# Performance work log

Hardware: AMD Instinct MI355X
Metric: run time of the kernel (lower is better)

The kernel has to match this reference:

```python
import jax, jax.numpy as jnp
import numpy as np

N_NODES = 100000


def _gcn_norm(edge_index, n):
    # PyG GCNConv: add self-loops, symmetric normalization D^-1/2 (A+I) D^-1/2
    loops = jnp.arange(n, dtype=edge_index.dtype)
    src = jnp.concatenate([edge_index[0], loops])
    dst = jnp.concatenate([edge_index[1], loops])
    deg = jax.ops.segment_sum(jnp.ones_like(dst, dtype=jnp.float32), dst, num_segments=n)
    dis = jnp.where(deg > 0, jax.lax.rsqrt(jnp.maximum(deg, 1.0)), 0.0)
    norm = dis[src] * dis[dst]  # [E + n]
    return src, dst, norm


def _gcn_layer(h, W, b, src, dst, norm, n):
    h = h @ W                              # dense projection [n, out]
    msg = h[src] * norm[:, None]           # gather + scale   [E+n, out]
    agg = jax.ops.segment_sum(msg, dst, num_segments=n)  # scatter-add
    return agg + b


def setup_inputs() -> dict:
    key = jax.random.key(0)
    ks = jax.random.split(key, 8)
    n, f, h, d, e = N_NODES, 256, 128, 64, 1600000
    x = jax.random.normal(ks[0], (n, f), dtype=jnp.float32)
    edge_index = jax.random.randint(ks[1], (2, e), 0, n, dtype=jnp.int64)
    s1 = 1.0 / np.sqrt(f)
    s2 = 1.0 / np.sqrt(h)
    return {
        "x": x,
        "edge_index": edge_index,
        "W1": jax.random.normal(ks[2], (f, h), dtype=jnp.float32) * s1,
        "b1": jnp.zeros((h,), dtype=jnp.float32),
        "Wmu": jax.random.normal(ks[3], (h, d), dtype=jnp.float32) * s2,
        "bmu": jnp.zeros((d,), dtype=jnp.float32),
        "Wvar": jax.random.normal(ks[4], (h, d), dtype=jnp.float32) * s2,
        "bvar": jnp.zeros((d,), dtype=jnp.float32),
    }


def reference(x, edge_index, W1, b1, Wmu, bmu, Wvar, bvar):
    n = x.shape[0]
    src, dst, norm = _gcn_norm(edge_index, n)
    h = jax.nn.relu(_gcn_layer(x, W1, b1, src, dst, norm, n))
    mu = _gcn_layer(h, Wmu, bmu, src, dst, norm, n)
    sigma = _gcn_layer(h, Wvar, bvar, src, dst, norm, n)
    return mu, sigma
```

## Files before the change

### kernel.cpp

```cpp
#include <hip/hip_runtime.h>


#define HID 128
#define DOUT 64
#define NB_SHIFT 8
#define CHUNK 8192
#define MAXNB 400

typedef _Float16 half_t;
typedef half_t f16x4 __attribute__((ext_vector_type(4)));
typedef half_t f16x8 __attribute__((ext_vector_type(8)));
typedef float  f32x4 __attribute__((ext_vector_type(4)));


__global__ __launch_bounds__(256) void bincount_kernel(const int* __restrict__ dst,
                                                       int* __restrict__ counts,
                                                       int E, int nblocks, int NB) {
    __shared__ int hist[MAXNB];
    const int b = blockIdx.x;
    for (int t = threadIdx.x; t < NB; t += 256) hist[t] = 0;
    __syncthreads();
    const int beg = b * CHUNK;
    const int end = min(E, beg + CHUNK);
    for (int e = beg + threadIdx.x; e < end; e += 256)
        atomicAdd(&hist[dst[e] >> NB_SHIFT], 1);
    __syncthreads();
    for (int t = threadIdx.x; t < NB; t += 256)
        counts[t * nblocks + b] = hist[t];
}

__global__ __launch_bounds__(256) void scan1_kernel(const int* __restrict__ in,
                                                    int* __restrict__ out,
                                                    int* __restrict__ bsum, int n) {
    __shared__ int s[256];
    int b = blockIdx.x, t = threadIdx.x;
    int base = b * 1024 + t * 4;
    int v0 = 0, v1 = 0, v2 = 0, v3 = 0;
    if (base + 0 < n) v0 = in[base + 0];
    if (base + 1 < n) v1 = in[base + 1];
    if (base + 2 < n) v2 = in[base + 2];
    if (base + 3 < n) v3 = in[base + 3];
    int tsum = v0 + v1 + v2 + v3;
    s[t] = tsum;
    __syncthreads();
    for (int off = 1; off < 256; off <<= 1) {
        int x = (t >= off) ? s[t - off] : 0;
        __syncthreads();
        s[t] += x;
        __syncthreads();
    }
    int excl = s[t] - tsum;
    if (base + 0 < n) out[base + 0] = excl;
    if (base + 1 < n) out[base + 1] = excl + v0;
    if (base + 2 < n) out[base + 2] = excl + v0 + v1;
    if (base + 3 < n) out[base + 3] = excl + v0 + v1 + v2;
    if (t == 255) bsum[b] = s[255];
}

__global__ __launch_bounds__(1024) void scan2_kernel(int* __restrict__ bsum, int nb) {
    __shared__ int s[1024];
    int t = threadIdx.x;
    int v = (t < nb) ? bsum[t] : 0;
    s[t] = v;
    __syncthreads();
    for (int off = 1; off < 1024; off <<= 1) {
        int x = (t >= off) ? s[t - off] : 0;
        __syncthreads();
        s[t] += x;
        __syncthreads();
    }
    if (t < nb) bsum[t] = s[t] - v;
}

__global__ void scan3_kernel(int* __restrict__ out, const int* __restrict__ bsum, int n) {
    int i = blockIdx.x * blockDim.x + threadIdx.x;
    if (i < n) out[i] += bsum[i >> 10];
}

__global__ __launch_bounds__(1024) void binscatter_kernel(const int* __restrict__ src,
                                                          const int* __restrict__ dst,
                                                          const int* __restrict__ offsets,
                                                          int2* __restrict__ binned,
                                                          int E, int nblocks, int NB) {
    __shared__ int  lhist[1024];
    __shared__ int  lbase[1024];
    __shared__ int  cur[1024];
    __shared__ int  goff[MAXNB];
    __shared__ int2 staged[CHUNK];
    const int b = blockIdx.x, t = threadIdx.x;
    const int beg = b * CHUNK;
    const int end = min(E, beg + CHUNK);
    const int ne  = end - beg;

    lhist[t] = 0;
    for (int k = t; k < NB; k += 1024) goff[k] = offsets[k * nblocks + b];
    __syncthreads();

    int2 regs[8];
    #pragma unroll
    for (int j = 0; j < 8; j++) {
        int e = beg + t + j * 1024;
        if (e < end) {
            regs[j] = make_int2(src[e], dst[e]);
            atomicAdd(&lhist[regs[j].y >> NB_SHIFT], 1);
        }
    }
    __syncthreads();

    int hv = lhist[t];
    for (int off = 1; off < 1024; off <<= 1) {
        int x = (t >= off) ? lhist[t - off] : 0;
        __syncthreads();
        lhist[t] += x;
        __syncthreads();
    }
    lbase[t] = lhist[t] - hv;
    cur[t]   = lhist[t] - hv;
    __syncthreads();

    #pragma unroll
    for (int j = 0; j < 8; j++) {
        int e = beg + t + j * 1024;
        if (e < end) {
            int pos = atomicAdd(&cur[regs[j].y >> NB_SHIFT], 1);
            staged[pos] = regs[j];
        }
    }
    __syncthreads();

    #pragma unroll
    for (int j = 0; j < 8; j++) {
        int tt = t + j * 1024;
        if (tt < ne) {
            int2 sd = staged[tt];
            int bkt = sd.y >> NB_SHIFT;
            binned[goff[bkt] + (tt - lbase[bkt])] = sd;
        }
    }
}

__global__ __launch_bounds__(256) void csrbuild_kernel(const int2* __restrict__ binned,
                                                       const int* __restrict__ offsets,
                                                       int* __restrict__ rowptr_end,
                                                       int* __restrict__ colA,
                                                       float* __restrict__ dis,
                                                       int E, int nblocks, int NB, int n) {
    __shared__ int deg[256];
    __shared__ int sc[256];
    __shared__ int cur[256];
    const int b = blockIdx.x;
    const int t = threadIdx.x;
    const int base = offsets[b * nblocks];
    const int bend = (b + 1 < NB) ? offsets[(b + 1) * nblocks] : E;

    deg[t] = 0;
    __syncthreads();
    for (int e = base + t; e < bend; e += 256)
        atomicAdd(&deg[binned[e].y & 255], 1);
    __syncthreads();

    int v = deg[t];
    sc[t] = v;
    __syncthreads();
    for (int off = 1; off < 256; off <<= 1) {
        int x = (t >= off) ? sc[t - off] : 0;
        __syncthreads();
        sc[t] += x;
        __syncthreads();
    }
    int incl = sc[t];
    int node = (b << NB_SHIFT) + t;
    if (node < n) {
        rowptr_end[node] = base + incl;
        dis[node] = rsqrtf((float)v + 1.0f);
    }
    cur[t] = base + incl - v;
    __syncthreads();

    for (int e = base + t; e < bend; e += 256) {
        int2 sd = binned[e];
        int pos = atomicAdd(&cur[sd.y & 255], 1);
        colA[pos] = sd.x;
    }
}

__global__ void w1t_kernel(const float* __restrict__ W1, half_t* __restrict__ W1T) {
    int i = blockIdx.x * blockDim.x + threadIdx.x;
    int k = i >> 7, nn = i & 127;
    W1T[nn * 256 + k] = (half_t)W1[i];
}
__global__ void wcatt_kernel(const float* __restrict__ Wmu, const float* __restrict__ Wvar,
                             half_t* __restrict__ WcatT) {
    int i = blockIdx.x * blockDim.x + threadIdx.x;
    int k = i >> 7, nn = i & 127;
    float v = (nn < DOUT) ? Wmu[k * DOUT + nn] : Wvar[k * DOUT + (nn - DOUT)];
    WcatT[nn * 128 + k] = (half_t)v;
}

__global__ __launch_bounds__(256) void gemm1_mfma(const float* __restrict__ A,
                                                  const half_t* __restrict__ BT,
                                                  const float* __restrict__ dis,
                                                  half_t* __restrict__ C, int M) {
    __shared__ half_t As[64][72];
    __shared__ half_t Bs[128][72];
    const int tid = threadIdx.x;
    const int block_row = blockIdx.x * 64;
    const int wave = tid >> 6, lane = tid & 63;
    const int wm = (wave & 1) * 32, wn = (wave >> 1) * 64;
    const int l16 = lane & 15, quad = lane >> 4;

    f32x4 acc[2][4] = {};
    float4 pa[4];
    f16x8  pb[4];

    #pragma unroll
    for (int i = 0; i < 4; i++) {
        int idx = tid + i * 256;
        int r = idx >> 4, c = idx & 15;
        int row = block_row + r; row = row < M ? row : M - 1;
        pa[i] = ((const float4*)(A + (size_t)row * 256))[c];
    }
    #pragma unroll
    for (int i = 0; i < 4; i++) {
        int idx = tid + i * 256;
        int nr = idx >> 3, kc = idx & 7;
        pb[i] = *(const f16x8*)(BT + (size_t)nr * 256 + kc * 8);
    }

    for (int k0 = 0; k0 < 256; k0 += 64) {
        #pragma unroll
        for (int i = 0; i < 4; i++) {
            int idx = tid + i * 256;
            int r = idx >> 4, c = idx & 15;
            f16x4 hv = { (half_t)pa[i].x, (half_t)pa[i].y, (half_t)pa[i].z, (half_t)pa[i].w };
            *(f16x4*)(&As[r][c * 4]) = hv;
        }
        #pragma unroll
        for (int i = 0; i < 4; i++) {
            int idx = tid + i * 256;
            int nr = idx >> 3, kc = idx & 7;
            *(f16x8*)(&Bs[nr][kc * 8]) = pb[i];
        }
        __syncthreads();

        if (k0 < 192) {
            #pragma unroll
            for (int i = 0; i < 4; i++) {
                int idx = tid + i * 256;
                int r = idx >> 4, c = idx & 15;
                int row = block_row + r; row = row < M ? row : M - 1;
                pa[i] = ((const float4*)(A + (size_t)row * 256 + k0 + 64))[c];
            }
            #pragma unroll
            for (int i = 0; i < 4; i++) {
                int idx = tid + i * 256;
                int nr = idx >> 3, kc = idx & 7;
                pb[i] = *(const f16x8*)(BT + (size_t)nr * 256 + k0 + 64 + kc * 8);
            }
        }

        #pragma unroll
        for (int ks = 0; ks < 2; ks++) {
            f16x8 af[2], bf[4];
            #pragma unroll
            for (int mt = 0; mt < 2; mt++)
                af[mt] = *(const f16x8*)(&As[wm + mt * 16 + l16][ks * 32 + quad * 8]);
            #pragma unroll
            for (int nt = 0; nt < 4; nt++)
                bf[nt] = *(const f16x8*)(&Bs[wn + nt * 16 + l16][ks * 32 + quad * 8]);
            #pragma unroll
            for (int mt = 0; mt < 2; mt++)
                #pragma unroll
                for (int nt = 0; nt < 4; nt++)
                    acc[mt][nt] = __builtin_amdgcn_mfma_f32_16x16x32_f16(af[mt], bf[nt], acc[mt][nt], 0, 0, 0);
        }
        __syncthreads();
    }

    #pragma unroll
    for (int mt = 0; mt < 2; mt++) {
        #pragma unroll
        for (int r = 0; r < 4; r++) {
            int row = block_row + wm + mt * 16 + quad * 4 + r;
            if (row < M) {
                float d = dis[row];
                #pragma unroll
                for (int nt = 0; nt < 4; nt++) {
                    int col = wn + nt * 16 + l16;
                    C[((size_t)(col >> 6) * M + row) * 64 + (col & 63)] = (half_t)(acc[mt][nt][r] * d);
                }
            }
        }
    }
}

__global__ __launch_bounds__(256) void gemm2_mfma(const half_t* __restrict__ A,
                                                  const half_t* __restrict__ BT,
                                                  const float* __restrict__ bmu,
                                                  const float* __restrict__ bvar,
                                                  float* __restrict__ out_mu,
                                                  float* __restrict__ out_sig, int M) {
    __shared__ half_t As[64][72];
    __shared__ half_t Bs[128][72];
    const int tid = threadIdx.x;
    const int block_row = blockIdx.x * 64;
    const int wave = tid >> 6, lane = tid & 63;
    const int wm = (wave & 1) * 32, wn = (wave >> 1) * 64;
    const int l16 = lane & 15, quad = lane >> 4;

    f32x4 acc[2][4] = {};
    f16x8 pa[2], pb[4];

    #pragma unroll
    for (int i = 0; i < 2; i++) {
        int idx = tid + i * 256;
        int r = idx >> 3, kc = idx & 7;
        int row = block_row + r; row = row < M ? row : M - 1;
        pa[i] = *(const f16x8*)(A + (size_t)row * 64 + kc * 8);
    }
    #pragma unroll
    for (int i = 0; i < 4; i++) {
        int idx = tid + i * 256;
        int nr = idx >> 3, kc = idx & 7;
        pb[i] = *(const f16x8*)(BT + (size_t)nr * 128 + kc * 8);
    }

    for (int k0 = 0; k0 < 128; k0 += 64) {
        #pragma unroll
        for (int i = 0; i < 2; i++) {
            int idx = tid + i * 256;
            int r = idx >> 3, kc = idx & 7;
            *(f16x8*)(&As[r][kc * 8]) = pa[i];
        }
        #pragma unroll
        for (int i = 0; i < 4; i++) {
            int idx = tid + i * 256;
            int nr = idx >> 3, kc = idx & 7;
            *(f16x8*)(&Bs[nr][kc * 8]) = pb[i];
        }
        __syncthreads();

        if (k0 < 64) {
            #pragma unroll
            for (int i = 0; i < 2; i++) {
                int idx = tid + i * 256;
                int r = idx >> 3, kc = idx & 7;
                int row = block_row + r; row = row < M ? row : M - 1;
                pa[i] = *(const f16x8*)(A + ((size_t)M + row) * 64 + kc * 8);
            }
            #pragma unroll
            for (int i = 0; i < 4; i++) {
                int idx = tid + i * 256;
                int nr = idx >> 3, kc = idx & 7;
                pb[i] = *(const f16x8*)(BT + (size_t)nr * 128 + 64 + kc * 8);
            }
        }

        #pragma unroll
        for (int ks = 0; ks < 2; ks++) {
            f16x8 af[2], bf[4];
            #pragma unroll
            for (int mt = 0; mt < 2; mt++)
                af[mt] = *(const f16x8*)(&As[wm + mt * 16 + l16][ks * 32 + quad * 8]);
            #pragma unroll
            for (int nt = 0; nt < 4; nt++)
                bf[nt] = *(const f16x8*)(&Bs[wn + nt * 16 + l16][ks * 32 + quad * 8]);
            #pragma unroll
            for (int mt = 0; mt < 2; mt++)
                #pragma unroll
                for (int nt = 0; nt < 4; nt++)
                    acc[mt][nt] = __builtin_amdgcn_mfma_f32_16x16x32_f16(af[mt], bf[nt], acc[mt][nt], 0, 0, 0);
        }
        __syncthreads();
    }

    float bias[4];
    int cols[4];
    #pragma unroll
    for (int nt = 0; nt < 4; nt++) {
        int col = wn + nt * 16 + l16;
        cols[nt] = col;
        bias[nt] = (col < DOUT) ? bmu[col] : bvar[col - DOUT];
    }

    #pragma unroll
    for (int mt = 0; mt < 2; mt++) {
        #pragma unroll
        for (int r = 0; r < 4; r++) {
            int row = block_row + wm + mt * 16 + quad * 4 + r;
            if (row < M) {
                #pragma unroll
                for (int nt = 0; nt < 4; nt++) {
                    int col = cols[nt];
                    float v = acc[mt][nt][r] + bias[nt];
                    if (col < DOUT) out_mu[(size_t)row * DOUT + col] = v;
                    else            out_sig[(size_t)row * DOUT + (col - DOUT)] = v;
                }
            }
        }
    }
}

__device__ __forceinline__ void acc_mix(float& a0, float& a1, float& a2, float& a3,
                                        f16x4 v, float fl) {
    union { f16x4 h; int i[2]; } u; u.h = v;
    asm("v_fma_mix_f32 %0, %1, %2, %0 op_sel_hi:[1,0,0]"
        : "+v"(a0) : "v"(u.i[0]), "v"(fl));
    asm("v_fma_mix_f32 %0, %1, %2, %0 op_sel:[1,0,0] op_sel_hi:[1,0,0]"
        : "+v"(a1) : "v"(u.i[0]), "v"(fl));
    asm("v_fma_mix_f32 %0, %1, %2, %0 op_sel_hi:[1,0,0]"
        : "+v"(a2) : "v"(u.i[1]), "v"(fl));
    asm("v_fma_mix_f32 %0, %1, %2, %0 op_sel:[1,0,0] op_sel_hi:[1,0,0]"
        : "+v"(a3) : "v"(u.i[1]), "v"(fl));
}

template <bool LAYER1>
__global__ __launch_bounds__(256) void agg_kernel(const int* __restrict__ rowptr_end,
                                                  const int* __restrict__ col,
                                                  const float* __restrict__ dis,
                                                  const half_t* __restrict__ hin,
                                                  half_t* __restrict__ hout,
                                                  const float* __restrict__ bias, int n) {
    const int bid   = blockIdx.x;
    const int chunk = (bid >> 2) & 1;
    const int nb4   = (bid >> 3) * 4 + (bid & 3);
    const int node  = nb4 * 16 + (threadIdx.x >> 4);
    if (node >= n) return;
    const int lane16 = threadIdx.x & 15;

    const f16x4* hc = (const f16x4*)(hin + (size_t)chunk * n * 64);

    int beg = (node == 0) ? 0 : rowptr_end[node - 1];
    int end = rowptr_end[node];

    float one = 1.0f;
    float ax = 0.f, ay = 0.f, az = 0.f, aw = 0.f;
    acc_mix(ax, ay, az, aw, hc[(size_t)node * 16 + lane16], one);

    int deg = end - beg;
    if (deg > 0) {
        const int last = end - 1;
        int c[8];
        #pragma unroll
        for (int j = 0; j < 8; j++) c[j] = col[min(beg + j, last)];

        int ng = (deg + 7) >> 3;
        int e = beg;
        for (int g = 0; g < ng; g++) {
            f16x4 v[8];
            #pragma unroll
            for (int j = 0; j < 8; j++) v[j] = hc[(size_t)c[j] * 16 + lane16];

            int enext = e + 8;
            if (g + 1 < ng) {
                #pragma unroll
                for (int j = 0; j < 8; j++) c[j] = col[min(enext + j, last)];
                #pragma unroll
                for (int j = 0; j < 8; j++) acc_mix(ax, ay, az, aw, v[j], one);
            } else {
                int rem = end - e;
                #pragma unroll
                for (int j = 0; j < 8; j++) {
                    float fl = (j < rem) ? 1.0f : 0.0f;
                    acc_mix(ax, ay, az, aw, v[j], fl);
                }
            }
            e = enext;
        }
    }

    float di = dis[node];
    if (LAYER1) {
        const float4 b = ((const float4*)bias)[chunk * 16 + lane16];
        ax = ax * di + b.x; ay = ay * di + b.y; az = az * di + b.z; aw = aw * di + b.w;
        ax = (ax > 0.f ? ax : 0.f) * di;
        ay = (ay > 0.f ? ay : 0.f) * di;
        az = (az > 0.f ? az : 0.f) * di;
        aw = (aw > 0.f ? aw : 0.f) * di;
    } else {
        ax *= di; ay *= di; az *= di; aw *= di;
    }
    f16x4 o = { (half_t)ax, (half_t)ay, (half_t)az, (half_t)aw };
    ((f16x4*)(hout + (size_t)chunk * n * 64))[(size_t)node * 16 + lane16] = o;
}

extern "C" void kernel_launch(void* const* d_in, const int* in_sizes, int n_in,
                              void* d_out, int out_size, void* d_ws, size_t ws_size,
                              hipStream_t stream) {
    const float* x    = (const float*)d_in[0];
    const int*   ei   = (const int*)d_in[1];
    const float* W1   = (const float*)d_in[2];
    const float* b1   = (const float*)d_in[3];
    const float* Wmu  = (const float*)d_in[4];
    const float* bmu  = (const float*)d_in[5];
    const float* Wvar = (const float*)d_in[6];
    const float* bvar = (const float*)d_in[7];

    const int n = in_sizes[0] / 256;
    const int E = in_sizes[1] / 2;
    const int* src = ei;
    const int* dst = ei + E;

    const int NB      = (n + 255) >> NB_SHIFT;
    const int nblocks = (E + CHUNK - 1) / CHUNK;
    const int flat    = NB * nblocks;
    const int nb_scan = (flat + 1023) / 1024;

    char* ws = (char*)d_ws;
    size_t off = 0;
    auto alloc = [&](size_t bytes) { void* p = ws + off; off = (off + bytes + 255) & ~(size_t)255; return p; };
    float*  dis     = (float*) alloc((size_t)n * 4);
    int*    rowptr  = (int*)   alloc((size_t)n * 4);
    int*    counts  = (int*)   alloc((size_t)flat * 4);
    int*    offsets = (int*)   alloc((size_t)flat * 4);
    int*    bsum    = (int*)   alloc((size_t)nb_scan * 4 + 256);
    int2*   binned  = (int2*)  alloc((size_t)E * 8);
    int*    col     = (int*)   alloc((size_t)E * 4);
    half_t* W1T     = (half_t*)alloc((size_t)256 * HID * 2);
    half_t* WcatT   = (half_t*)alloc((size_t)HID * HID * 2);
    half_t* hs      = (half_t*)alloc((size_t)n * HID * 2);
    half_t* h1s     = (half_t*)alloc((size_t)n * HID * 2);
    half_t* agg2    = hs;

    float* out_mu  = (float*)d_out;
    float* out_sig = (float*)d_out + (size_t)n * DOUT;

    bincount_kernel<<<nblocks, 256, 0, stream>>>(dst, counts, E, nblocks, NB);
    scan1_kernel<<<nb_scan, 256, 0, stream>>>(counts, offsets, bsum, flat);
    scan2_kernel<<<1, 1024, 0, stream>>>(bsum, nb_scan);
    scan3_kernel<<<(flat + 255) / 256, 256, 0, stream>>>(offsets, bsum, flat);
    binscatter_kernel<<<nblocks, 1024, 0, stream>>>(src, dst, offsets, binned, E, nblocks, NB);
    csrbuild_kernel<<<NB, 256, 0, stream>>>(binned, offsets, rowptr, col, dis, E, nblocks, NB, n);

    w1t_kernel<<<(256 * HID) / 256, 256, 0, stream>>>(W1, W1T);
    wcatt_kernel<<<(HID * HID) / 256, 256, 0, stream>>>(Wmu, Wvar, WcatT);

    const int aggGrid = ((n + 63) / 64) * 8;
    gemm1_mfma<<<(n + 63) / 64, 256, 0, stream>>>(x, W1T, dis, hs, n);
    agg_kernel<true><<<aggGrid, 256, 0, stream>>>(rowptr, col, dis, hs, h1s, b1, n);
    agg_kernel<false><<<aggGrid, 256, 0, stream>>>(rowptr, col, dis, h1s, agg2, nullptr, n);
    gemm2_mfma<<<(n + 63) / 64, 256, 0, stream>>>(agg2, WcatT, bmu, bvar, out_mu, out_sig, n);
}
```

Measured before the change: 198.7 us.

## Widen aggregation loads to 16 bytes and fold scan/weight-prep launches

The aggregation kernel now has each thread handle 8 half features with 16-byte loads instead of 4 with 8-byte loads, so each 64-feature chunk row is covered by 8 lanes and a block covers 32 nodes instead of 16. The aim is fewer memory transactions per gathered neighbor row and fewer threads issuing per edge. The scan3 fix-up kernel is removed, and the block-sum correction is applied where the offsets are read in binscatter and csrbuild. The two weight-transpose kernels are merged into one launch. Per-thread register use grows with the 8-wide accumulators and loads, which could lower occupancy for the latency-bound gather.

```diff
diff --git a/kernel.cpp b/kernel.cpp
--- a/kernel.cpp
+++ b/kernel.cpp
@@ -72,14 +72,10 @@
     if (t < nb) bsum[t] = s[t] - v;
 }
 
-__global__ void scan3_kernel(int* __restrict__ out, const int* __restrict__ bsum, int n) {
-    int i = blockIdx.x * blockDim.x + threadIdx.x;
-    if (i < n) out[i] += bsum[i >> 10];
-}
-
 __global__ __launch_bounds__(1024) void binscatter_kernel(const int* __restrict__ src,
                                                           const int* __restrict__ dst,
                                                           const int* __restrict__ offsets,
+                                                          const int* __restrict__ bsum,
                                                           int2* __restrict__ binned,
                                                           int E, int nblocks, int NB) {
     __shared__ int  lhist[1024];
@@ -93,7 +89,10 @@
     const int ne  = end - beg;
 
     lhist[t] = 0;
-    for (int k = t; k < NB; k += 1024) goff[k] = offsets[k * nblocks + b];
+    for (int k = t; k < NB; k += 1024) {
+        int idx = k * nblocks + b;
+        goff[k] = offsets[idx] + bsum[idx >> 10];
+    }
     __syncthreads();
 
     int2 regs[8];
@@ -141,6 +140,7 @@
 
 __global__ __launch_bounds__(256) void csrbuild_kernel(const int2* __restrict__ binned,
                                                        const int* __restrict__ offsets,
+                                                       const int* __restrict__ bsum,
                                                        int* __restrict__ rowptr_end,
                                                        int* __restrict__ colA,
                                                        float* __restrict__ dis,
@@ -150,8 +150,11 @@
     __shared__ int cur[256];
     const int b = blockIdx.x;
     const int t = threadIdx.x;
-    const int base = offsets[b * nblocks];
-    const int bend = (b + 1 < NB) ? offsets[(b + 1) * nblocks] : E;
+    const int i0 = b * nblocks;
+    const int base = offsets[i0] + bsum[i0 >> 10];
+    int bend;
+    if (b + 1 < NB) { int i1 = (b + 1) * nblocks; bend = offsets[i1] + bsum[i1 >> 10]; }
+    else            bend = E;
 
     deg[t] = 0;
     __syncthreads();
@@ -184,17 +187,21 @@
     }
 }
 
-__global__ void w1t_kernel(const float* __restrict__ W1, half_t* __restrict__ W1T) {
-    int i = blockIdx.x * blockDim.x + threadIdx.x;
-    int k = i >> 7, nn = i & 127;
-    W1T[nn * 256 + k] = (half_t)W1[i];
-}
-__global__ void wcatt_kernel(const float* __restrict__ Wmu, const float* __restrict__ Wvar,
+__global__ void wprep_kernel(const float* __restrict__ W1,
+                             const float* __restrict__ Wmu,
+                             const float* __restrict__ Wvar,
+                             half_t* __restrict__ W1T,
                              half_t* __restrict__ WcatT) {
     int i = blockIdx.x * blockDim.x + threadIdx.x;
-    int k = i >> 7, nn = i & 127;
-    float v = (nn < DOUT) ? Wmu[k * DOUT + nn] : Wvar[k * DOUT + (nn - DOUT)];
-    WcatT[nn * 128 + k] = (half_t)v;
+    if (i < 256 * HID) {
+        int k = i >> 7, nn = i & 127;
+        W1T[nn * 256 + k] = (half_t)W1[i];
+    } else {
+        int j = i - 256 * HID;
+        int k = j >> 7, nn = j & 127;
+        float v = (nn < DOUT) ? Wmu[k * DOUT + nn] : Wvar[k * DOUT + (nn - DOUT)];
+        WcatT[nn * 128 + k] = (half_t)v;
+    }
 }
 
 __global__ __launch_bounds__(256) void gemm1_mfma(const float* __restrict__ A,
@@ -401,17 +408,15 @@
     }
 }
 
-__device__ __forceinline__ void acc_mix(float& a0, float& a1, float& a2, float& a3,
-                                        f16x4 v, float fl) {
-    union { f16x4 h; int i[2]; } u; u.h = v;
-    asm("v_fma_mix_f32 %0, %1, %2, %0 op_sel_hi:[1,0,0]"
-        : "+v"(a0) : "v"(u.i[0]), "v"(fl));
-    asm("v_fma_mix_f32 %0, %1, %2, %0 op_sel:[1,0,0] op_sel_hi:[1,0,0]"
-        : "+v"(a1) : "v"(u.i[0]), "v"(fl));
-    asm("v_fma_mix_f32 %0, %1, %2, %0 op_sel_hi:[1,0,0]"
-        : "+v"(a2) : "v"(u.i[1]), "v"(fl));
-    asm("v_fma_mix_f32 %0, %1, %2, %0 op_sel:[1,0,0] op_sel_hi:[1,0,0]"
-        : "+v"(a3) : "v"(u.i[1]), "v"(fl));
+__device__ __forceinline__ void acc_mix8(float* a, f16x8 v, float fl) {
+    union { f16x8 h; int i[4]; } u; u.h = v;
+    #pragma unroll
+    for (int k = 0; k < 4; k++) {
+        asm("v_fma_mix_f32 %0, %1, %2, %0 op_sel_hi:[1,0,0]"
+            : "+v"(a[2 * k]) : "v"(u.i[k]), "v"(fl));
+        asm("v_fma_mix_f32 %0, %1, %2, %0 op_sel:[1,0,0] op_sel_hi:[1,0,0]"
+            : "+v"(a[2 * k + 1]) : "v"(u.i[k]), "v"(fl));
+    }
 }
 
 template <bool LAYER1>
@@ -423,19 +428,19 @@
                                                   const float* __restrict__ bias, int n) {
     const int bid   = blockIdx.x;
     const int chunk = (bid >> 2) & 1;
-    const int nb4   = (bid >> 3) * 4 + (bid & 3);
-    const int node  = nb4 * 16 + (threadIdx.x >> 4);
+    const int nb    = (bid >> 3) * 4 + (bid & 3);
+    const int node  = nb * 32 + (threadIdx.x >> 3);
     if (node >= n) return;
-    const int lane16 = threadIdx.x & 15;
-
-    const f16x4* hc = (const f16x4*)(hin + (size_t)chunk * n * 64);
+    const int lane8 = threadIdx.x & 7;
+
+    const f16x8* hc = (const f16x8*)(hin + (size_t)chunk * n * 64);
 
     int beg = (node == 0) ? 0 : rowptr_end[node - 1];
     int end = rowptr_end[node];
 
     float one = 1.0f;
-    float ax = 0.f, ay = 0.f, az = 0.f, aw = 0.f;
-    acc_mix(ax, ay, az, aw, hc[(size_t)node * 16 + lane16], one);
+    float a[8] = {};
+    acc_mix8(a, hc[(size_t)node * 8 + lane8], one);
 
     int deg = end - beg;
     if (deg > 0) {
@@ -447,22 +452,22 @@
         int ng = (deg + 7) >> 3;
         int e = beg;
         for (int g = 0; g < ng; g++) {
-            f16x4 v[8];
-            #pragma unroll
-            for (int j = 0; j < 8; j++) v[j] = hc[(size_t)c[j] * 16 + lane16];
+            f16x8 v[8];
+            #pragma unroll
+            for (int j = 0; j < 8; j++) v[j] = hc[(size_t)c[j] * 8 + lane8];
 
             int enext = e + 8;
             if (g + 1 < ng) {
                 #pragma unroll
                 for (int j = 0; j < 8; j++) c[j] = col[min(enext + j, last)];
                 #pragma unroll
-                for (int j = 0; j < 8; j++) acc_mix(ax, ay, az, aw, v[j], one);
+                for (int j = 0; j < 8; j++) acc_mix8(a, v[j], one);
             } else {
                 int rem = end - e;
                 #pragma unroll
                 for (int j = 0; j < 8; j++) {
                     float fl = (j < rem) ? 1.0f : 0.0f;
-                    acc_mix(ax, ay, az, aw, v[j], fl);
+                    acc_mix8(a, v[j], fl);
                 }
             }
             e = enext;
@@ -471,17 +476,21 @@
 
     float di = dis[node];
     if (LAYER1) {
-        const float4 b = ((const float4*)bias)[chunk * 16 + lane16];
-        ax = ax * di + b.x; ay = ay * di + b.y; az = az * di + b.z; aw = aw * di + b.w;
-        ax = (ax > 0.f ? ax : 0.f) * di;
-        ay = (ay > 0.f ? ay : 0.f) * di;
-        az = (az > 0.f ? az : 0.f) * di;
-        aw = (aw > 0.f ? aw : 0.f) * di;
+        const float4 b0 = ((const float4*)bias)[chunk * 16 + lane8 * 2];
+        const float4 b1 = ((const float4*)bias)[chunk * 16 + lane8 * 2 + 1];
+        float bb[8] = { b0.x, b0.y, b0.z, b0.w, b1.x, b1.y, b1.z, b1.w };
+        #pragma unroll
+        for (int k = 0; k < 8; k++) {
+            float t = a[k] * di + bb[k];
+            a[k] = (t > 0.f ? t : 0.f) * di;
+        }
     } else {
-        ax *= di; ay *= di; az *= di; aw *= di;
-    }
-    f16x4 o = { (half_t)ax, (half_t)ay, (half_t)az, (half_t)aw };
-    ((f16x4*)(hout + (size_t)chunk * n * 64))[(size_t)node * 16 + lane16] = o;
+        #pragma unroll
+        for (int k = 0; k < 8; k++) a[k] *= di;
+    }
+    f16x8 o = { (half_t)a[0], (half_t)a[1], (half_t)a[2], (half_t)a[3],
+                (half_t)a[4], (half_t)a[5], (half_t)a[6], (half_t)a[7] };
+    ((f16x8*)(hout + (size_t)chunk * n * 64))[(size_t)node * 8 + lane8] = o;
 }
 
 extern "C" void kernel_launch(void* const* d_in, const int* in_sizes, int n_in,
@@ -528,14 +537,12 @@
     bincount_kernel<<<nblocks, 256, 0, stream>>>(dst, counts, E, nblocks, NB);
     scan1_kernel<<<nb_scan, 256, 0, stream>>>(counts, offsets, bsum, flat);
     scan2_kernel<<<1, 1024, 0, stream>>>(bsum, nb_scan);
-    scan3_kernel<<<(flat + 255) / 256, 256, 0, stream>>>(offsets, bsum, flat);
-    binscatter_kernel<<<nblocks, 1024, 0, stream>>>(src, dst, offsets, binned, E, nblocks, NB);
-    csrbuild_kernel<<<NB, 256, 0, stream>>>(binned, offsets, rowptr, col, dis, E, nblocks, NB, n);
-
-    w1t_kernel<<<(256 * HID) / 256, 256, 0, stream>>>(W1, W1T);
-    wcatt_kernel<<<(HID * HID) / 256, 256, 0, stream>>>(Wmu, Wvar, WcatT);
-
-    const int aggGrid = ((n + 63) / 64) * 8;
+    binscatter_kernel<<<nblocks, 1024, 0, stream>>>(src, dst, offsets, bsum, binned, E, nblocks, NB);
+    csrbuild_kernel<<<NB, 256, 0, stream>>>(binned, offsets, bsum, rowptr, col, dis, E, nblocks, NB, n);
+
+    wprep_kernel<<<(256 * HID + HID * HID) / 256, 256, 0, stream>>>(W1, Wmu, Wvar, W1T, WcatT);
+
+    const int aggGrid = ((n + 127) / 128) * 8;
     gemm1_mfma<<<(n + 63) / 64, 256, 0, stream>>>(x, W1T, dis, hs, n);
     agg_kernel<true><<<aggGrid, 256, 0, stream>>>(rowptr, col, dis, hs, h1s, b1, n);
     agg_kernel<false><<<aggGrid, 256, 0, stream>>>(rowptr, col, dis, h1s, agg2, nullptr, n);
```

After: 193.2 us. -2.8%, faster.
